# Kernel tuning notes

Hardware: AMD Instinct MI355X
Metric: run time of the kernel (lower is better)

## Reference

```python
import jax, jax.numpy as jnp
import numpy as np

N_GROUPS = 32  # getGroupSize(.) assumed -> channels // 8 (or //24 for 3*ch) == 32 for ch=256
HEADS = 4


def group_norm(x, gamma, beta, groups=N_GROUPS, eps=1e-5):
    n, c = x.shape
    xg = x.reshape(n, groups, c // groups)
    mu = xg.mean(-1, keepdims=True)
    var = xg.var(-1, keepdims=True)
    xn = ((xg - mu) * jax.lax.rsqrt(var + eps)).reshape(n, c)
    return xn * gamma + beta


def setup_inputs():
    key = jax.random.key(0)
    N, E, CH, HID = 2000, 16000, 256, 256
    ks = jax.random.split(key, 24)

    def w(k, shape, s=0.02):
        return (jax.random.normal(k, shape) * s).astype(jnp.float32)

    inp = {
        'x': jax.random.normal(ks[0], (N, CH), jnp.float32),
        'edge_index': jax.random.randint(ks[1], (2, E), 0, N),
        'edge_attr': jax.random.normal(ks[2], (E, CH), jnp.float32),
        # edge_mlp: GN(3ch)+ReLU -> Linear(3ch,hid) -> GN(hid)+ReLU -> Linear(hid,ch)
        'gn_e1_g': jnp.ones((3 * CH,), jnp.float32), 'gn_e1_b': jnp.zeros((3 * CH,), jnp.float32),
        'We1': w(ks[3], (3 * CH, HID)), 'be1': jnp.zeros((HID,), jnp.float32),
        'gn_e2_g': jnp.ones((HID,), jnp.float32), 'gn_e2_b': jnp.zeros((HID,), jnp.float32),
        'We2': w(ks[4], (HID, CH)), 'be2': jnp.zeros((CH,), jnp.float32),
        # actN: GN(ch)+ReLU
        'gn_n_g': jnp.ones((CH,), jnp.float32), 'gn_n_b': jnp.zeros((CH,), jnp.float32),
        # multi-head attention projections
        'Wq': w(ks[5], (CH, CH)), 'bq': jnp.zeros((CH,), jnp.float32),
        'Wk': w(ks[6], (CH, CH)), 'bk': jnp.zeros((CH,), jnp.float32),
        'Wv': w(ks[7], (CH, CH)), 'bv': jnp.zeros((CH,), jnp.float32),
        'Wo': w(ks[8], (CH, CH)), 'bo': jnp.zeros((CH,), jnp.float32),
        # node_mlp: Linear(2ch,hid) -> GN(hid)+ReLU -> Linear(hid,ch)
        'Wn1': w(ks[9], (2 * CH, HID)), 'bn1': jnp.zeros((HID,), jnp.float32),
        'gn_n2_g': jnp.ones((HID,), jnp.float32), 'gn_n2_b': jnp.zeros((HID,), jnp.float32),
        'Wn2': w(ks[10], (HID, CH)), 'bn2': jnp.zeros((CH,), jnp.float32),
    }
    return inp


def reference(x, edge_index, edge_attr,
              gn_e1_g, gn_e1_b, We1, be1, gn_e2_g, gn_e2_b, We2, be2,
              gn_n_g, gn_n_b, Wq, bq, Wk, bk, Wv, bv, Wo, bo,
              Wn1, bn1, gn_n2_g, gn_n2_b, Wn2, bn2):
    row, col = edge_index[0], edge_index[1]
    N, ch = x.shape
    E = edge_attr.shape[0]
    dk = ch // HEADS

    # ---- edge model: cat(src, tgt, e) -> GN/ReLU -> Lin -> GN/ReLU -> Lin (+res) ----
    e_in = jnp.concatenate([x[row], x[col], edge_attr], axis=1)  # [E, 3ch]
    h = jax.nn.relu(group_norm(e_in, gn_e1_g, gn_e1_b))
    h = h @ We1 + be1
    h = jax.nn.relu(group_norm(h, gn_e2_g, gn_e2_b))
    e_out = h @ We2 + be2 + edge_attr  # [E, ch]

    # ---- node model: dense-masked MHA, queries=nodes, keys/values=edges ----
    mask = jnp.zeros((N, E), x.dtype).at[col, jnp.arange(E)].set(1.0)  # scatter adjacency
    q = (x @ Wq + bq).reshape(N, HEADS, dk)
    k = (e_out @ Wk + bk).reshape(E, HEADS, dk)
    v = (e_out @ Wv + bv).reshape(E, HEADS, dk)
    scores = jnp.einsum('nhd,ehd->hne', q, k) / jnp.sqrt(jnp.float32(dk))  # [H, N, E]
    scores = jnp.where(mask[None] > 0, scores, jnp.float32(-1e9))
    attn = jax.nn.softmax(scores, axis=-1)
    g = jnp.einsum('hne,ehd->nhd', attn, v).reshape(N, ch) @ Wo + bo  # [N, ch]

    xa = jax.nn.relu(group_norm(x, gn_n_g, gn_n_b))
    h = jnp.concatenate([xa, g], axis=1) @ Wn1 + bn1  # thinker='cat'
    h = jax.nn.relu(group_norm(h, gn_n2_g, gn_n2_b))
    n_out = h @ Wn2 + bn2 + x  # residual

    return n_out, e_out
```

## Files before the change

### kernel.cpp

```cpp
#include <hip/hip_runtime.h>
#include <hip/hip_bf16.h>
#include <stdint.h>
#include <math.h>

#define CH 256

typedef __attribute__((ext_vector_type(8)))  short short8;
typedef __attribute__((ext_vector_type(16))) short short16;
typedef __attribute__((ext_vector_type(4)))  float f32x4;

#define GL2LDS16(g, l) __builtin_amdgcn_global_load_lds(                       \
    (const __attribute__((address_space(1))) void*)(g),                        \
    (__attribute__((address_space(3))) void*)(l), 16, 0, 0)

__device__ inline short f2bf(float f) {
    __hip_bfloat16 h = __float2bfloat16(f);
    short s;
    __builtin_memcpy(&s, &h, 2);
    return s;
}

__device__ inline float warp_sum64(float v) {
    v += __shfl_xor(v, 32, 64);
    v += __shfl_xor(v, 16, 64);
    v += __shfl_xor(v, 8, 64);
    v += __shfl_xor(v, 4, 64);
    v += __shfl_xor(v, 2, 64);
    v += __shfl_xor(v, 1, 64);
    return v;
}

__device__ inline float warp_max64(float v) {
    v = fmaxf(v, __shfl_xor(v, 32, 64));
    v = fmaxf(v, __shfl_xor(v, 16, 64));
    v = fmaxf(v, __shfl_xor(v, 8, 64));
    v = fmaxf(v, __shfl_xor(v, 4, 64));
    v = fmaxf(v, __shfl_xor(v, 2, 64));
    v = fmaxf(v, __shfl_xor(v, 1, 64));
    return v;
}

template <int BM, int BN, int EPI, int VB>
__global__ __launch_bounds__(256) void mfma_gemm(
    const short* __restrict__ A, const short* __restrict__ Bt,
    const float* __restrict__ bias, const float* __restrict__ res,
    float* __restrict__ C, short* __restrict__ Cbf,
    const float* __restrict__ gamma, const float* __restrict__ beta,
    float* __restrict__ vbar,
    int M, int K, int Nc, int ldc, int coff)
{
    constexpr int BK = 64;
    constexpr int HM = BM / 2, HN = BN / 2;
    constexpr int FM = HM / 16, FN = HN / 16;
    constexpr int PA = (BM * BK) / (256 * 8);
    constexpr int PB = (BN * BK) / (256 * 8);
    __shared__ short As[BM * BK];
    __shared__ short Bs[BN * BK];

    const int t = threadIdx.x;
    const int wave = t >> 6, lane = t & 63;
    const int q = lane >> 4, l16 = lane & 15;
    const int row0 = blockIdx.y * BM;
    const int col0 = blockIdx.x * BN;
    const int wm = wave & 1, wn = wave >> 1;

    f32x4 acc[FM][FN];
    #pragma unroll
    for (int i = 0; i < FM; i++)
        #pragma unroll
        for (int j = 0; j < FN; j++) acc[i][j] = (f32x4){0.f, 0.f, 0.f, 0.f};

    for (int k0 = 0; k0 < K; k0 += BK) {
        #pragma unroll
        for (int p = 0; p < PA; p++) {
            int chunk = p * 256 + t;
            int r = chunk >> 3, ko = (chunk & 7) * 8;
            int gr = row0 + r; if (gr >= M) gr = M - 1;
            const short* gsrc = A + (size_t)gr * K + k0 + ko;
            short* ldst = &As[(p * 256 + wave * 64) * 8];
            GL2LDS16(gsrc, ldst);
        }
        #pragma unroll
        for (int p = 0; p < PB; p++) {
            int chunk = p * 256 + t;
            int r = chunk >> 3, ko = (chunk & 7) * 8;
            const short* gsrc = Bt + (size_t)(col0 + r) * K + k0 + ko;
            short* ldst = &Bs[(p * 256 + wave * 64) * 8];
            GL2LDS16(gsrc, ldst);
        }
        __syncthreads();
        #pragma unroll
        for (int ks = 0; ks < 2; ks++) {
            short8 af[FM], bf[FN];
            #pragma unroll
            for (int mi = 0; mi < FM; mi++)
                af[mi] = *(const short8*)&As[(wm * HM + mi * 16 + l16) * BK + ks * 32 + q * 8];
            #pragma unroll
            for (int ni = 0; ni < FN; ni++)
                bf[ni] = *(const short8*)&Bs[(wn * HN + ni * 16 + l16) * BK + ks * 32 + q * 8];
            #pragma unroll
            for (int mi = 0; mi < FM; mi++)
                #pragma unroll
                for (int ni = 0; ni < FN; ni++)
                    acc[mi][ni] = __builtin_amdgcn_mfma_f32_16x16x32_bf16(
                        af[mi], bf[ni], acc[mi][ni], 0, 0, 0);
        }
        __syncthreads();
    }

    #pragma unroll
    for (int ni = 0; ni < FN; ni++) {
        int cg = col0 + wn * HN + ni * 16 + l16;
        float bv = bias[cg];
        if constexpr (EPI == 1) {
            float ga = gamma[cg], be = beta[cg];
            #pragma unroll
            for (int mi = 0; mi < FM; mi++) {
                #pragma unroll
                for (int r = 0; r < 4; r++) {
                    float v = acc[mi][ni][r] + bv;
                    float s = v, sq = v * v;
                    s += __shfl_xor(s, 1, 64);  sq += __shfl_xor(sq, 1, 64);
                    s += __shfl_xor(s, 2, 64);  sq += __shfl_xor(sq, 2, 64);
                    s += __shfl_xor(s, 4, 64);  sq += __shfl_xor(sq, 4, 64);
                    float mean = s * 0.125f;
                    float var = sq * 0.125f - mean * mean;
                    float o = fmaxf((v - mean) * rsqrtf(var + 1e-5f) * ga + be, 0.f);
                    int rg = row0 + wm * HM + mi * 16 + q * 4 + r;
                    if (rg < M) Cbf[(size_t)rg * ldc + coff + cg] = f2bf(o);
                }
            }
        } else {
            #pragma unroll
            for (int mi = 0; mi < FM; mi++) {
                #pragma unroll
                for (int r = 0; r < 4; r++) {
                    int rg = row0 + wm * HM + mi * 16 + q * 4 + r;
                    if (rg < M) {
                        float v = acc[mi][ni][r] + bv;
                        if (res) v += res[(size_t)rg * ldc + coff + cg];
                        if (C)   C[(size_t)rg * ldc + coff + cg] = v;
                        if (Cbf) Cbf[(size_t)rg * ldc + coff + cg] = f2bf(v);
                    }
                }
            }
            if constexpr (VB) {
                if (cg >= 256) {
                    float part = 0.f;
                    #pragma unroll
                    for (int mi = 0; mi < FM; mi++)
                        #pragma unroll
                        for (int r = 0; r < 4; r++) {
                            int rg = row0 + wm * HM + mi * 16 + q * 4 + r;
                            if (rg < M) part += acc[mi][ni][r] + bv;
                        }
                    part += __shfl_xor(part, 16, 64);
                    part += __shfl_xor(part, 32, 64);
                    if (q == 0) atomicAdd(&vbar[cg - 256], part);
                }
            }
        }
    }
}

struct PrepPack {
    const float* wsrc[8];
    short* wdst[8];
    int wK[8];
    int wstart[8];
    int NW, NP;
    const float* x;
    short* x_bf;
    short* cat_bf;
    const float* gng;
    const float* gnb;
    float* vbar;
    const float* bk;
    const float* bv;
    float* bkv;
    int* counts;
    int N;
};

__global__ __launch_bounds__(256) void prep_kernel(PrepPack p)
{
    int bid = blockIdx.x;
    int t = threadIdx.x;
    if (bid < p.NW) {
        int m = 0;
        #pragma unroll
        for (int i = 1; i < 8; i++) if (bid >= p.wstart[i]) m = i;
        int k0 = (bid - p.wstart[m]) * 16;
        const float* src = p.wsrc[m];
        short16 o;
        #pragma unroll
        for (int j = 0; j < 16; j++) o[j] = f2bf(src[(size_t)(k0 + j) * 256 + t]);
        *(short16*)(p.wdst[m] + (size_t)t * p.wK[m] + k0) = o;
        return;
    }
    if (bid >= p.NW + p.NP) {
        int i = (bid - p.NW - p.NP) * 256 + t;
        if (i < p.N) p.counts[i] = 0;
        return;
    }
    int pb = bid - p.NW;
    if (pb == 0) {
        p.vbar[t] = 0.f;
        p.bkv[t] = p.bk[t];
        p.bkv[256 + t] = p.bv[t];
    }
    int r = pb * 8 + (t >> 5);
    int g = t & 31;
    if (r >= p.N) return;
    size_t xb = (size_t)r * CH + g * 8;
    float4 a = *(const float4*)&p.x[xb];
    float4 b = *(const float4*)&p.x[xb + 4];
    short8 xr;
    xr[0] = f2bf(a.x); xr[1] = f2bf(a.y); xr[2] = f2bf(a.z); xr[3] = f2bf(a.w);
    xr[4] = f2bf(b.x); xr[5] = f2bf(b.y); xr[6] = f2bf(b.z); xr[7] = f2bf(b.w);
    *(short8*)&p.x_bf[xb] = xr;
    float s  = a.x + a.y + a.z + a.w + b.x + b.y + b.z + b.w;
    float s2 = a.x*a.x + a.y*a.y + a.z*a.z + a.w*a.w
             + b.x*b.x + b.y*b.y + b.z*b.z + b.w*b.w;
    float m = s * 0.125f;
    float var = s2 * 0.125f - m * m;
    float rsd = rsqrtf(var + 1e-5f);
    float4 g0 = *(const float4*)&p.gng[g * 8];
    float4 g1 = *(const float4*)&p.gng[g * 8 + 4];
    float4 b0 = *(const float4*)&p.gnb[g * 8];
    float4 b1 = *(const float4*)&p.gnb[g * 8 + 4];
    short8 o;
    o[0] = f2bf(fmaxf((a.x - m) * rsd * g0.x + b0.x, 0.f));
    o[1] = f2bf(fmaxf((a.y - m) * rsd * g0.y + b0.y, 0.f));
    o[2] = f2bf(fmaxf((a.z - m) * rsd * g0.z + b0.z, 0.f));
    o[3] = f2bf(fmaxf((a.w - m) * rsd * g0.w + b0.w, 0.f));
    o[4] = f2bf(fmaxf((b.x - m) * rsd * g1.x + b1.x, 0.f));
    o[5] = f2bf(fmaxf((b.y - m) * rsd * g1.y + b1.y, 0.f));
    o[6] = f2bf(fmaxf((b.z - m) * rsd * g1.z + b1.z, 0.f));
    o[7] = f2bf(fmaxf((b.w - m) * rsd * g1.w + b1.w, 0.f));
    *(short8*)&p.cat_bf[(size_t)r * (2 * CH) + g * 8] = o;
}

__global__ __launch_bounds__(256) void build_ein_kernel(
    const float* __restrict__ x, const float* __restrict__ eattr,
    const int* __restrict__ rowi, const int* __restrict__ coli,
    const float* __restrict__ gng, const float* __restrict__ gnb,
    short* __restrict__ ein, int* __restrict__ counts, int E)
{
    __shared__ float sb[768];
    __shared__ float smu[32], srs[32];
    int e = blockIdx.x, t = threadIdx.x;
    int r = rowi[e], c = coli[e];
    if (t == 0) atomicAdd(&counts[c], 1);
    float v0 = x[(size_t)r * CH + t];
    float v1 = x[(size_t)c * CH + t];
    float v2 = eattr[(size_t)e * CH + t];
    sb[t] = v0; sb[256 + t] = v1; sb[512 + t] = v2;
    __syncthreads();
    if (t < 32) {
        float s = 0.f, s2 = 0.f;
        const float* p = &sb[t * 24];
        #pragma unroll
        for (int i = 0; i < 24; i++) { float v = p[i]; s += v; s2 += v * v; }
        float m = s * (1.f / 24.f);
        float var = s2 * (1.f / 24.f) - m * m;
        smu[t] = m; srs[t] = rsqrtf(var + 1e-5f);
    }
    __syncthreads();
    size_t base = (size_t)e * 768;
    #pragma unroll
    for (int j = 0; j < 3; j++) {
        int pos = j * 256 + t;
        int g = pos / 24;
        float v = (j == 0) ? v0 : (j == 1) ? v1 : v2;
        v = fmaxf((v - smu[g]) * srs[g] * gng[pos] + gnb[pos], 0.f);
        ein[base + pos] = f2bf(v);
    }
}

__global__ __launch_bounds__(1024) void scan_kernel(
    const int* __restrict__ counts, int* __restrict__ offsets,
    int* __restrict__ cursor, int N)
{
    __shared__ int s[1024];
    int t = threadIdx.x;
    int a = (2 * t     < N) ? counts[2 * t]     : 0;
    int b = (2 * t + 1 < N) ? counts[2 * t + 1] : 0;
    s[t] = a + b;
    __syncthreads();
    for (int off = 1; off < 1024; off <<= 1) {
        int v = (t >= off) ? s[t - off] : 0;
        __syncthreads();
        s[t] += v;
        __syncthreads();
    }
    int excl = (t > 0) ? s[t - 1] : 0;
    if (2 * t < N)     { offsets[2 * t]     = excl;     cursor[2 * t]     = excl; }
    if (2 * t + 1 < N) { offsets[2 * t + 1] = excl + a; cursor[2 * t + 1] = excl + a; }
    if (t == 1023) offsets[N] = s[1023];
}

__global__ void fill_kernel(const int* __restrict__ coli, int* __restrict__ cursor,
                            int* __restrict__ elist, int E)
{
    int e = blockIdx.x * blockDim.x + threadIdx.x;
    if (e < E) {
        int p = atomicAdd(&cursor[coli[e]], 1);
        elist[p] = e;
    }
}

__global__ __launch_bounds__(256) void escore_kernel(
    const float* __restrict__ qb, const float* __restrict__ kv,
    const int* __restrict__ coli, float* __restrict__ sc, int E)
{
    int e = blockIdx.x * 4 + (threadIdx.x >> 6);
    int lane = threadIdx.x & 63;
    if (e >= E) return;
    int c = coli[e];
    const float* qrow = qb + (size_t)c * CH;
    const float* krow = kv + (size_t)e * 512;
    float d0 = qrow[lane]       * krow[lane];
    float d1 = qrow[64 + lane]  * krow[64 + lane];
    float d2 = qrow[128 + lane] * krow[128 + lane];
    float d3 = qrow[192 + lane] * krow[192 + lane];
    d0 = warp_sum64(d0);
    d1 = warp_sum64(d1);
    d2 = warp_sum64(d2);
    d3 = warp_sum64(d3);
    if (lane == 0) {
        float4 o = {d0 * 0.125f, d1 * 0.125f, d2 * 0.125f, d3 * 0.125f};
        *(float4*)&sc[(size_t)e * 4] = o;
    }
}

__global__ __launch_bounds__(256) void attn_kernel(
    const float* __restrict__ sc, const float* __restrict__ kv,
    const int* __restrict__ offsets, const int* __restrict__ elist,
    const float* __restrict__ vbar, short* __restrict__ g_bf, int N, int E)
{
    int n = blockIdx.x;
    int h = threadIdx.x >> 6;
    int lane = threadIdx.x & 63;
    int s0 = offsets[n], s1 = offsets[n + 1];
    float out = 0.f;
    if (s1 > s0) {
        float m = -INFINITY, l = 0.f;
        for (int base = s0; base < s1; base += 64) {
            int cn = s1 - base; if (cn > 64) cn = 64;
            int e = (lane < cn) ? elist[base + lane] : 0;
            float s = (lane < cn) ? sc[(size_t)e * 4 + h] : -INFINITY;
            float mc = warp_max64(s);
            float nm = fmaxf(m, mc);
            float scale = __expf(m - nm);
            float pp = (lane < cn) ? __expf(s - nm) : 0.f;
            float ps = warp_sum64(pp);
            l = l * scale + ps;
            out *= scale;
            m = nm;
            for (int i = 0; i < cn; i++) {
                float pi = __shfl(pp, i, 64);
                int   ei = __shfl(e, i, 64);
                out += pi * kv[(size_t)ei * 512 + 256 + h * 64 + lane];
            }
        }
        out /= l;
    } else {
        out = vbar[h * 64 + lane] * (1.f / (float)E);
    }
    g_bf[(size_t)n * CH + h * 64 + lane] = f2bf(out);
}

extern "C" void kernel_launch(void* const* d_in, const int* in_sizes, int n_in,
                              void* d_out, int out_size, void* d_ws, size_t ws_size,
                              hipStream_t stream)
{
    const float* x       = (const float*)d_in[0];
    const int*   ei      = (const int*)d_in[1];
    const float* eattr   = (const float*)d_in[2];
    const float* gn_e1_g = (const float*)d_in[3];
    const float* gn_e1_b = (const float*)d_in[4];
    const float* We1     = (const float*)d_in[5];
    const float* be1     = (const float*)d_in[6];
    const float* gn_e2_g = (const float*)d_in[7];
    const float* gn_e2_b = (const float*)d_in[8];
    const float* We2     = (const float*)d_in[9];
    const float* be2     = (const float*)d_in[10];
    const float* gn_n_g  = (const float*)d_in[11];
    const float* gn_n_b  = (const float*)d_in[12];
    const float* Wq      = (const float*)d_in[13];
    const float* bq      = (const float*)d_in[14];
    const float* Wk      = (const float*)d_in[15];
    const float* bk      = (const float*)d_in[16];
    const float* Wv      = (const float*)d_in[17];
    const float* bv      = (const float*)d_in[18];
    const float* Wo      = (const float*)d_in[19];
    const float* bo      = (const float*)d_in[20];
    const float* Wn1     = (const float*)d_in[21];
    const float* bn1     = (const float*)d_in[22];
    const float* gn_n2_g = (const float*)d_in[23];
    const float* gn_n2_b = (const float*)d_in[24];
    const float* Wn2     = (const float*)d_in[25];
    const float* bn2     = (const float*)d_in[26];

    const int N = in_sizes[0] / CH;
    const int E = in_sizes[2] / CH;

    float* nout = (float*)d_out;
    float* eout = (float*)d_out + (size_t)N * CH;

    char* base = (char*)d_ws;
    short* ein_bf = (short*)base;
    float* kvbuf  = (float*)base;
    base += (size_t)E * 512 * 4;
    short* h2_bf  = (short*)base; base += (size_t)E * CH * 2;
    short* eo_bf  = (short*)base; base += (size_t)E * CH * 2;
    float* qbuf   = (float*)base; base += (size_t)N * CH * 4;
    short* g_bf   = (short*)base; base += (size_t)N * CH * 2;
    short* cat_bf = (short*)base; base += (size_t)N * 2 * CH * 2;
    short* hn_bf  = (short*)base; base += (size_t)N * CH * 2;
    short* x_bf   = (short*)base; base += (size_t)N * CH * 2;
    float* sc     = (float*)base; base += (size_t)E * 4 * 4;
    float* vbar   = (float*)base; base += 1024;
    float* bkv    = (float*)base; base += 2048;
    short* We1t = (short*)base; base += (size_t)768 * 256 * 2;
    short* We2t = (short*)base; base += (size_t)256 * 256 * 2;
    short* Wqt  = (short*)base; base += (size_t)256 * 256 * 2;
    short* Wkvt = (short*)base; base += (size_t)512 * 256 * 2;
    short* Wot  = (short*)base; base += (size_t)256 * 256 * 2;
    short* Wn1t = (short*)base; base += (size_t)512 * 256 * 2;
    short* Wn2t = (short*)base; base += (size_t)256 * 256 * 2;
    int* counts  = (int*)base;
    int* offsets = counts + N;
    int* cursor  = offsets + (N + 1) + 3;
    int* elist   = cursor + N;

    const int* rowi = ei;
    const int* coli = ei + E;

    dim3 blk(256);
    dim3 gE(CH / 64, E / 128);
    dim3 gKV(512 / 128, E / 128);
    dim3 gN(CH / 64, (N + 63) / 64);

    PrepPack pp;
    const float* wsrc[8] = {We1, We2, Wq, Wk, Wv, Wo, Wn1, Wn2};
    short* wdst[8] = {We1t, We2t, Wqt, Wkvt, Wkvt + (size_t)256 * 256, Wot, Wn1t, Wn2t};
    const int wKd[8] = {768, 256, 256, 256, 256, 256, 512, 256};
    int acc = 0;
    for (int i = 0; i < 8; i++) {
        pp.wsrc[i] = wsrc[i]; pp.wdst[i] = wdst[i]; pp.wK[i] = wKd[i];
        pp.wstart[i] = acc; acc += wKd[i] / 16;
    }
    pp.NW = acc;
    pp.NP = (N + 7) / 8;
    pp.x = x; pp.x_bf = x_bf; pp.cat_bf = cat_bf;
    pp.gng = gn_n_g; pp.gnb = gn_n_b;
    pp.vbar = vbar; pp.bk = bk; pp.bv = bv; pp.bkv = bkv;
    pp.counts = counts; pp.N = N;
    int nzero = (N + 255) / 256;
    prep_kernel<<<pp.NW + pp.NP + nzero, blk, 0, stream>>>(pp);

    build_ein_kernel<<<E, blk, 0, stream>>>(x, eattr, rowi, coli, gn_e1_g, gn_e1_b,
                                            ein_bf, counts, E);
    scan_kernel<<<1, 1024, 0, stream>>>(counts, offsets, cursor, N);
    fill_kernel<<<(E + 255) / 256, blk, 0, stream>>>(coli, cursor, elist, E);

    mfma_gemm<128, 64, 1, 0><<<gE, blk, 0, stream>>>(
        ein_bf, We1t, be1, nullptr, nullptr, h2_bf, gn_e2_g, gn_e2_b, nullptr,
        E, 3 * CH, CH, CH, 0);
    mfma_gemm<128, 64, 0, 0><<<gE, blk, 0, stream>>>(
        h2_bf, We2t, be2, eattr, eout, eo_bf, nullptr, nullptr, nullptr,
        E, CH, CH, CH, 0);

    mfma_gemm<128, 128, 0, 1><<<gKV, blk, 0, stream>>>(
        eo_bf, Wkvt, bkv, nullptr, kvbuf, nullptr, nullptr, nullptr, vbar,
        E, CH, 512, 512, 0);
    mfma_gemm<64, 64, 0, 0><<<gN, blk, 0, stream>>>(
        x_bf, Wqt, bq, nullptr, qbuf, nullptr, nullptr, nullptr, nullptr,
        N, CH, CH, CH, 0);

    escore_kernel<<<(E + 3) / 4, blk, 0, stream>>>(qbuf, kvbuf, coli, sc, E);
    attn_kernel<<<N, blk, 0, stream>>>(sc, kvbuf, offsets, elist, vbar, g_bf, N, E);
    mfma_gemm<64, 64, 0, 0><<<gN, blk, 0, stream>>>(
        g_bf, Wot, bo, nullptr, nullptr, cat_bf, nullptr, nullptr, nullptr,
        N, CH, CH, 2 * CH, CH);

    mfma_gemm<64, 64, 1, 0><<<gN, blk, 0, stream>>>(
        cat_bf, Wn1t, bn1, nullptr, nullptr, hn_bf, gn_n2_g, gn_n2_b, nullptr,
        N, 2 * CH, CH, CH, 0);
    mfma_gemm<64, 64, 0, 0><<<gN, blk, 0, stream>>>(
        hn_bf, Wn2t, bn2, x, nout, nullptr, nullptr, nullptr, nullptr,
        N, CH, CH, CH, 0);
}
```

Measured before the change: 267.2 us.

## Fuse edge GroupNorm gather into GEMM A-load, merge Q/KV GEMMs, store KV/Q as bf16

Removes the materialised [E,768] bf16 edge-input buffer. Per-group statistics are now computed from precomputed node partial sums plus edge sums, and the first edge GEMM gathers x rows and eattr, normalizes them and writes the result to LDS itself. The Q and KV projections run as one dual-role launch, and Q/KV are stored in bf16 instead of fp32. The fill kernel is folded into escore. All GEMMs now use 128x128 tiles. This saves memory traffic and launches, but the A tile is now built by a register path instead of async LDS loads, bf16 Q/K adds precision loss, and small-N GEMMs get fewer blocks.

Result: slower. 342.0 us (+28.0%).

```diff
diff --git a/kernel.cpp b/kernel.cpp
--- a/kernel.cpp
+++ b/kernel.cpp
@@ -18,6 +18,13 @@
     short s;
     __builtin_memcpy(&s, &h, 2);
     return s;
+}
+
+__device__ inline float bf2f(short s) {
+    unsigned u = ((unsigned)(unsigned short)s) << 16;
+    float f;
+    __builtin_memcpy(&f, &u, 4);
+    return f;
 }
 
 __device__ inline float warp_sum64(float v) {
@@ -40,48 +47,114 @@
     return v;
 }
 
-template <int BM, int BN, int EPI, int VB>
-__global__ __launch_bounds__(256) void mfma_gemm(
-    const short* __restrict__ A, const short* __restrict__ Bt,
-    const float* __restrict__ bias, const float* __restrict__ res,
-    float* __restrict__ C, short* __restrict__ Cbf,
-    const float* __restrict__ gamma, const float* __restrict__ beta,
-    float* __restrict__ vbar,
-    int M, int K, int Nc, int ldc, int coff)
-{
-    constexpr int BK = 64;
-    constexpr int HM = BM / 2, HN = BN / 2;
-    constexpr int FM = HM / 16, FN = HN / 16;
-    constexpr int PA = (BM * BK) / (256 * 8);
-    constexpr int PB = (BN * BK) / (256 * 8);
-    __shared__ short As[BM * BK];
+struct GArgs {
+    const short* A; const short* Bt; const float* bias; const float* res;
+    float* C; short* Cbf;
+    const float* gamma; const float* beta; float* vbar;
+    int M, K, Nc, ldc, coff;
+    const short* A2; const short* Bt2; const float* bias2; short* Cbf2;
+    int M2, Nc2, y_split;
+    const float* x; const float* eattr; const int* rowi; const int* coli;
+    const float* mu; const float* rs; const float* vg; const float* vbt;
+};
+
+template <int AMODE, int EPI, int DUAL, int VB>
+__global__ __launch_bounds__(256) void mfma_gemm(GArgs g)
+{
+    constexpr int BM = 128, BN = 128, BK = 64;
+    constexpr int AK = AMODE ? (BK + 8) : BK;
+    __shared__ short As[BM * AK];
     __shared__ short Bs[BN * BK];
+    __shared__ int sidx[AMODE ? 256 : 1];
+
+    const short* A = g.A; const short* Bt = g.Bt;
+    const float* bias = g.bias; const float* res = g.res;
+    float* C = g.C; short* Cbf = g.Cbf;
+    int M = g.M, ldc = g.ldc, co = g.coff;
+    const int K = g.K;
+    int by = blockIdx.y, bx = blockIdx.x;
+    bool qrole = false;
+    if constexpr (DUAL) {
+        if (by >= g.y_split) {
+            by -= g.y_split;
+            if (bx * BN >= g.Nc2) return;
+            qrole = true;
+            A = g.A2; Bt = g.Bt2; bias = g.bias2; Cbf = g.Cbf2;
+            C = nullptr; res = nullptr;
+            M = g.M2; ldc = g.Nc2; co = 0;
+        }
+    }
 
     const int t = threadIdx.x;
     const int wave = t >> 6, lane = t & 63;
     const int q = lane >> 4, l16 = lane & 15;
-    const int row0 = blockIdx.y * BM;
-    const int col0 = blockIdx.x * BN;
+    const int row0 = by * BM;
+    const int col0 = bx * BN;
     const int wm = wave & 1, wn = wave >> 1;
 
-    f32x4 acc[FM][FN];
+    if constexpr (AMODE) {
+        if (t < 128) {
+            int gr = row0 + t; if (gr >= M) gr = M - 1;
+            sidx[t] = g.rowi[gr];
+            sidx[128 + t] = g.coli[gr];
+        }
+        __syncthreads();
+    }
+
+    f32x4 acc[4][4];
     #pragma unroll
-    for (int i = 0; i < FM; i++)
+    for (int i = 0; i < 4; i++)
         #pragma unroll
-        for (int j = 0; j < FN; j++) acc[i][j] = (f32x4){0.f, 0.f, 0.f, 0.f};
+        for (int j = 0; j < 4; j++) acc[i][j] = (f32x4){0.f, 0.f, 0.f, 0.f};
 
     for (int k0 = 0; k0 < K; k0 += BK) {
+        if constexpr (AMODE == 1) {
+            int reg = k0 >> 8;
+            int rloc = t >> 3;
+            int cpos = (t & 7) * 8;
+            int pos = k0 + cpos;
+            int G = pos / 24;
+            float4 ga  = *(const float4*)&g.vg[pos];
+            float4 ga2 = *(const float4*)&g.vg[pos + 4];
+            float4 gb  = *(const float4*)&g.vbt[pos];
+            float4 gb2 = *(const float4*)&g.vbt[pos + 4];
+            int off = pos & 255;
+            #pragma unroll
+            for (int p = 0; p < 4; p++) {
+                int rr2 = p * 32 + rloc;
+                int e = row0 + rr2; if (e >= M) e = M - 1;
+                const float* srow;
+                if (reg == 0)      srow = g.x + (size_t)sidx[rr2] * CH;
+                else if (reg == 1) srow = g.x + (size_t)sidx[128 + rr2] * CH;
+                else               srow = g.eattr + (size_t)e * CH;
+                float4 va = *(const float4*)&srow[off];
+                float4 vb4 = *(const float4*)&srow[off + 4];
+                float mm = g.mu[(size_t)e * 32 + G];
+                float rr = g.rs[(size_t)e * 32 + G];
+                short8 o;
+                o[0] = f2bf(fmaxf((va.x - mm) * rr * ga.x + gb.x, 0.f));
+                o[1] = f2bf(fmaxf((va.y - mm) * rr * ga.y + gb.y, 0.f));
+                o[2] = f2bf(fmaxf((va.z - mm) * rr * ga.z + gb.z, 0.f));
+                o[3] = f2bf(fmaxf((va.w - mm) * rr * ga.w + gb.w, 0.f));
+                o[4] = f2bf(fmaxf((vb4.x - mm) * rr * ga2.x + gb2.x, 0.f));
+                o[5] = f2bf(fmaxf((vb4.y - mm) * rr * ga2.y + gb2.y, 0.f));
+                o[6] = f2bf(fmaxf((vb4.z - mm) * rr * ga2.z + gb2.z, 0.f));
+                o[7] = f2bf(fmaxf((vb4.w - mm) * rr * ga2.w + gb2.w, 0.f));
+                *(short8*)&As[rr2 * AK + cpos] = o;
+            }
+        } else {
+            #pragma unroll
+            for (int p = 0; p < 4; p++) {
+                int chunk = p * 256 + t;
+                int r = chunk >> 3, ko = (chunk & 7) * 8;
+                int gr = row0 + r; if (gr >= M) gr = M - 1;
+                const short* gsrc = A + (size_t)gr * K + k0 + ko;
+                short* ldst = &As[(p * 256 + wave * 64) * 8];
+                GL2LDS16(gsrc, ldst);
+            }
+        }
         #pragma unroll
-        for (int p = 0; p < PA; p++) {
-            int chunk = p * 256 + t;
-            int r = chunk >> 3, ko = (chunk & 7) * 8;
-            int gr = row0 + r; if (gr >= M) gr = M - 1;
-            const short* gsrc = A + (size_t)gr * K + k0 + ko;
-            short* ldst = &As[(p * 256 + wave * 64) * 8];
-            GL2LDS16(gsrc, ldst);
-        }
-        #pragma unroll
-        for (int p = 0; p < PB; p++) {
+        for (int p = 0; p < 4; p++) {
             int chunk = p * 256 + t;
             int r = chunk >> 3, ko = (chunk & 7) * 8;
             const short* gsrc = Bt + (size_t)(col0 + r) * K + k0 + ko;
@@ -91,17 +164,17 @@
         __syncthreads();
         #pragma unroll
         for (int ks = 0; ks < 2; ks++) {
-            short8 af[FM], bf[FN];
-            #pragma unroll
-            for (int mi = 0; mi < FM; mi++)
-                af[mi] = *(const short8*)&As[(wm * HM + mi * 16 + l16) * BK + ks * 32 + q * 8];
-            #pragma unroll
-            for (int ni = 0; ni < FN; ni++)
-                bf[ni] = *(const short8*)&Bs[(wn * HN + ni * 16 + l16) * BK + ks * 32 + q * 8];
-            #pragma unroll
-            for (int mi = 0; mi < FM; mi++)
+            short8 af[4], bf[4];
+            #pragma unroll
+            for (int mi = 0; mi < 4; mi++)
+                af[mi] = *(const short8*)&As[(wm * 64 + mi * 16 + l16) * AK + ks * 32 + q * 8];
+            #pragma unroll
+            for (int ni = 0; ni < 4; ni++)
+                bf[ni] = *(const short8*)&Bs[(wn * 64 + ni * 16 + l16) * BK + ks * 32 + q * 8];
+            #pragma unroll
+            for (int mi = 0; mi < 4; mi++)
                 #pragma unroll
-                for (int ni = 0; ni < FN; ni++)
+                for (int ni = 0; ni < 4; ni++)
                     acc[mi][ni] = __builtin_amdgcn_mfma_f32_16x16x32_bf16(
                         af[mi], bf[ni], acc[mi][ni], 0, 0, 0);
         }
@@ -109,13 +182,13 @@
     }
 
     #pragma unroll
-    for (int ni = 0; ni < FN; ni++) {
-        int cg = col0 + wn * HN + ni * 16 + l16;
+    for (int ni = 0; ni < 4; ni++) {
+        int cg = col0 + wn * 64 + ni * 16 + l16;
         float bv = bias[cg];
         if constexpr (EPI == 1) {
-            float ga = gamma[cg], be = beta[cg];
-            #pragma unroll
-            for (int mi = 0; mi < FM; mi++) {
+            float ga = g.gamma[cg], be = g.beta[cg];
+            #pragma unroll
+            for (int mi = 0; mi < 4; mi++) {
                 #pragma unroll
                 for (int r = 0; r < 4; r++) {
                     float v = acc[mi][ni][r] + bv;
@@ -126,37 +199,37 @@
                     float mean = s * 0.125f;
                     float var = sq * 0.125f - mean * mean;
                     float o = fmaxf((v - mean) * rsqrtf(var + 1e-5f) * ga + be, 0.f);
-                    int rg = row0 + wm * HM + mi * 16 + q * 4 + r;
-                    if (rg < M) Cbf[(size_t)rg * ldc + coff + cg] = f2bf(o);
+                    int rg = row0 + wm * 64 + mi * 16 + q * 4 + r;
+                    if (rg < M) Cbf[(size_t)rg * ldc + co + cg] = f2bf(o);
                 }
             }
         } else {
             #pragma unroll
-            for (int mi = 0; mi < FM; mi++) {
+            for (int mi = 0; mi < 4; mi++) {
                 #pragma unroll
                 for (int r = 0; r < 4; r++) {
-                    int rg = row0 + wm * HM + mi * 16 + q * 4 + r;
+                    int rg = row0 + wm * 64 + mi * 16 + q * 4 + r;
                     if (rg < M) {
                         float v = acc[mi][ni][r] + bv;
-                        if (res) v += res[(size_t)rg * ldc + coff + cg];
-                        if (C)   C[(size_t)rg * ldc + coff + cg] = v;
-                        if (Cbf) Cbf[(size_t)rg * ldc + coff + cg] = f2bf(v);
+                        if (res) v += res[(size_t)rg * ldc + co + cg];
+                        if (C)   C[(size_t)rg * ldc + co + cg] = v;
+                        if (Cbf) Cbf[(size_t)rg * ldc + co + cg] = f2bf(v);
                     }
                 }
             }
             if constexpr (VB) {
-                if (cg >= 256) {
+                if (!qrole && cg >= 256) {
                     float part = 0.f;
                     #pragma unroll
-                    for (int mi = 0; mi < FM; mi++)
+                    for (int mi = 0; mi < 4; mi++)
                         #pragma unroll
                         for (int r = 0; r < 4; r++) {
-                            int rg = row0 + wm * HM + mi * 16 + q * 4 + r;
+                            int rg = row0 + wm * 64 + mi * 16 + q * 4 + r;
                             if (rg < M) part += acc[mi][ni][r] + bv;
                         }
                     part += __shfl_xor(part, 16, 64);
                     part += __shfl_xor(part, 32, 64);
-                    if (q == 0) atomicAdd(&vbar[cg - 256], part);
+                    if (q == 0) atomicAdd(&g.vbar[cg - 256], part);
                 }
             }
         }
@@ -172,6 +245,7 @@
     const float* x;
     short* x_bf;
     short* cat_bf;
+    float2* xs;
     const float* gng;
     const float* gnb;
     float* vbar;
@@ -222,6 +296,7 @@
     float s  = a.x + a.y + a.z + a.w + b.x + b.y + b.z + b.w;
     float s2 = a.x*a.x + a.y*a.y + a.z*a.z + a.w*a.w
              + b.x*b.x + b.y*b.y + b.z*b.z + b.w*b.w;
+    p.xs[(size_t)r * 32 + g] = make_float2(s, s2);
     float m = s * 0.125f;
     float var = s2 * 0.125f - m * m;
     float rsd = rsqrtf(var + 1e-5f);
@@ -241,41 +316,40 @@
     *(short8*)&p.cat_bf[(size_t)r * (2 * CH) + g * 8] = o;
 }
 
-__global__ __launch_bounds__(256) void build_ein_kernel(
-    const float* __restrict__ x, const float* __restrict__ eattr,
-    const int* __restrict__ rowi, const int* __restrict__ coli,
-    const float* __restrict__ gng, const float* __restrict__ gnb,
-    short* __restrict__ ein, int* __restrict__ counts, int E)
-{
-    __shared__ float sb[768];
-    __shared__ float smu[32], srs[32];
-    int e = blockIdx.x, t = threadIdx.x;
+__global__ __launch_bounds__(256) void estats_kernel(
+    const float* __restrict__ eattr, const int* __restrict__ rowi,
+    const int* __restrict__ coli, const float2* __restrict__ xs,
+    float* __restrict__ mu, float* __restrict__ rs,
+    int* __restrict__ counts, int E)
+{
+    __shared__ float2 ea[8][32];
+    int t = threadIdx.x;
+    int slot = t >> 5, g = t & 31;
+    int e = blockIdx.x * 8 + slot;
+    float4 a = *(const float4*)&eattr[(size_t)e * CH + g * 8];
+    float4 b = *(const float4*)&eattr[(size_t)e * CH + g * 8 + 4];
+    float s  = a.x + a.y + a.z + a.w + b.x + b.y + b.z + b.w;
+    float s2 = a.x*a.x + a.y*a.y + a.z*a.z + a.w*a.w
+             + b.x*b.x + b.y*b.y + b.z*b.z + b.w*b.w;
+    ea[slot][g] = make_float2(s, s2);
     int r = rowi[e], c = coli[e];
-    if (t == 0) atomicAdd(&counts[c], 1);
-    float v0 = x[(size_t)r * CH + t];
-    float v1 = x[(size_t)c * CH + t];
-    float v2 = eattr[(size_t)e * CH + t];
-    sb[t] = v0; sb[256 + t] = v1; sb[512 + t] = v2;
+    if (g == 0) atomicAdd(&counts[c], 1);
     __syncthreads();
-    if (t < 32) {
-        float s = 0.f, s2 = 0.f;
-        const float* p = &sb[t * 24];
-        #pragma unroll
-        for (int i = 0; i < 24; i++) { float v = p[i]; s += v; s2 += v * v; }
-        float m = s * (1.f / 24.f);
-        float var = s2 * (1.f / 24.f) - m * m;
-        smu[t] = m; srs[t] = rsqrtf(var + 1e-5f);
-    }
-    __syncthreads();
-    size_t base = (size_t)e * 768;
+    float S = 0.f, S2 = 0.f;
     #pragma unroll
     for (int j = 0; j < 3; j++) {
-        int pos = j * 256 + t;
-        int g = pos / 24;
-        float v = (j == 0) ? v0 : (j == 1) ? v1 : v2;
-        v = fmaxf((v - smu[g]) * srs[g] * gng[pos] + gnb[pos], 0.f);
-        ein[base + pos] = f2bf(v);
-    }
+        int b3 = 3 * g + j;
+        int src = b3 >> 5, idx = b3 & 31;
+        float2 v;
+        if (src == 0)      v = xs[(size_t)r * 32 + idx];
+        else if (src == 1) v = xs[(size_t)c * 32 + idx];
+        else               v = ea[slot][idx];
+        S += v.x; S2 += v.y;
+    }
+    float m = S * (1.f / 24.f);
+    float var = S2 * (1.f / 24.f) - m * m;
+    mu[(size_t)e * 32 + g] = m;
+    rs[(size_t)e * 32 + g] = rsqrtf(var + 1e-5f);
 }
 
 __global__ __launch_bounds__(1024) void scan_kernel(
@@ -300,30 +374,22 @@
     if (t == 1023) offsets[N] = s[1023];
 }
 
-__global__ void fill_kernel(const int* __restrict__ coli, int* __restrict__ cursor,
-                            int* __restrict__ elist, int E)
-{
-    int e = blockIdx.x * blockDim.x + threadIdx.x;
-    if (e < E) {
-        int p = atomicAdd(&cursor[coli[e]], 1);
-        elist[p] = e;
-    }
-}
-
 __global__ __launch_bounds__(256) void escore_kernel(
-    const float* __restrict__ qb, const float* __restrict__ kv,
-    const int* __restrict__ coli, float* __restrict__ sc, int E)
+    const short* __restrict__ qb, const short* __restrict__ kvb,
+    const int* __restrict__ coli, int* __restrict__ cursor,
+    int* __restrict__ elist, float* __restrict__ sc, int E)
 {
     int e = blockIdx.x * 4 + (threadIdx.x >> 6);
     int lane = threadIdx.x & 63;
     if (e >= E) return;
     int c = coli[e];
-    const float* qrow = qb + (size_t)c * CH;
-    const float* krow = kv + (size_t)e * 512;
-    float d0 = qrow[lane]       * krow[lane];
-    float d1 = qrow[64 + lane]  * krow[64 + lane];
-    float d2 = qrow[128 + lane] * krow[128 + lane];
-    float d3 = qrow[192 + lane] * krow[192 + lane];
+    if (lane == 0) { int p = atomicAdd(&cursor[c], 1); elist[p] = e; }
+    const short* qrow = qb + (size_t)c * CH;
+    const short* krow = kvb + (size_t)e * 512;
+    float d0 = bf2f(qrow[lane])       * bf2f(krow[lane]);
+    float d1 = bf2f(qrow[64 + lane])  * bf2f(krow[64 + lane]);
+    float d2 = bf2f(qrow[128 + lane]) * bf2f(krow[128 + lane]);
+    float d3 = bf2f(qrow[192 + lane]) * bf2f(krow[192 + lane]);
     d0 = warp_sum64(d0);
     d1 = warp_sum64(d1);
     d2 = warp_sum64(d2);
@@ -335,7 +401,7 @@
 }
 
 __global__ __launch_bounds__(256) void attn_kernel(
-    const float* __restrict__ sc, const float* __restrict__ kv,
+    const float* __restrict__ sc, const short* __restrict__ kvb,
     const int* __restrict__ offsets, const int* __restrict__ elist,
     const float* __restrict__ vbar, short* __restrict__ g_bf, int N, int E)
 {
@@ -361,7 +427,7 @@
             for (int i = 0; i < cn; i++) {
                 float pi = __shfl(pp, i, 64);
                 int   ei = __shfl(e, i, 64);
-                out += pi * kv[(size_t)ei * 512 + 256 + h * 64 + lane];
+                out += pi * bf2f(kvb[(size_t)ei * 512 + 256 + h * 64 + lane]);
             }
         }
         out /= l;
@@ -410,16 +476,17 @@
     float* eout = (float*)d_out + (size_t)N * CH;
 
     char* base = (char*)d_ws;
-    short* ein_bf = (short*)base;
-    float* kvbuf  = (float*)base;
-    base += (size_t)E * 512 * 4;
+    short* kv_bf  = (short*)base; base += (size_t)E * 512 * 2;
     short* h2_bf  = (short*)base; base += (size_t)E * CH * 2;
     short* eo_bf  = (short*)base; base += (size_t)E * CH * 2;
-    float* qbuf   = (float*)base; base += (size_t)N * CH * 4;
+    short* q_bf   = (short*)base; base += (size_t)N * CH * 2;
     short* g_bf   = (short*)base; base += (size_t)N * CH * 2;
     short* cat_bf = (short*)base; base += (size_t)N * 2 * CH * 2;
     short* hn_bf  = (short*)base; base += (size_t)N * CH * 2;
     short* x_bf   = (short*)base; base += (size_t)N * CH * 2;
+    float2* xs    = (float2*)base; base += (size_t)N * 32 * 8;
+    float* mub    = (float*)base; base += (size_t)E * 32 * 4;
+    float* rsb    = (float*)base; base += (size_t)E * 32 * 4;
     float* sc     = (float*)base; base += (size_t)E * 4 * 4;
     float* vbar   = (float*)base; base += 1024;
     float* bkv    = (float*)base; base += 2048;
@@ -439,9 +506,6 @@
     const int* coli = ei + E;
 
     dim3 blk(256);
-    dim3 gE(CH / 64, E / 128);
-    dim3 gKV(512 / 128, E / 128);
-    dim3 gN(CH / 64, (N + 63) / 64);
 
     PrepPack pp;
     const float* wsrc[8] = {We1, We2, Wq, Wk, Wv, Wo, Wn1, Wn2};
@@ -454,42 +518,53 @@
     }
     pp.NW = acc;
     pp.NP = (N + 7) / 8;
-    pp.x = x; pp.x_bf = x_bf; pp.cat_bf = cat_bf;
+    pp.x = x; pp.x_bf = x_bf; pp.cat_bf = cat_bf; pp.xs = xs;
     pp.gng = gn_n_g; pp.gnb = gn_n_b;
     pp.vbar = vbar; pp.bk = bk; pp.bv = bv; pp.bkv = bkv;
     pp.counts = counts; pp.N = N;
     int nzero = (N + 255) / 256;
     prep_kernel<<<pp.NW + pp.NP + nzero, blk, 0, stream>>>(pp);
 
-    build_ein_kernel<<<E, blk, 0, stream>>>(x, eattr, rowi, coli, gn_e1_g, gn_e1_b,
-                                            ein_bf, counts, E);
+    estats_kernel<<<E / 8, blk, 0, stream>>>(eattr, rowi, coli, xs, mub, rsb, counts, E);
     scan_kernel<<<1, 1024, 0, stream>>>(counts, offsets, cursor, N);
-    fill_kernel<<<(E + 255) / 256, blk, 0, stream>>>(coli, cursor, elist, E);
-
-    mfma_gemm<128, 64, 1, 0><<<gE, blk, 0, stream>>>(
-        ein_bf, We1t, be1, nullptr, nullptr, h2_bf, gn_e2_g, gn_e2_b, nullptr,
-        E, 3 * CH, CH, CH, 0);
-    mfma_gemm<128, 64, 0, 0><<<gE, blk, 0, stream>>>(
-        h2_bf, We2t, be2, eattr, eout, eo_bf, nullptr, nullptr, nullptr,
-        E, CH, CH, CH, 0);
-
-    mfma_gemm<128, 128, 0, 1><<<gKV, blk, 0, stream>>>(
-        eo_bf, Wkvt, bkv, nullptr, kvbuf, nullptr, nullptr, nullptr, vbar,
-        E, CH, 512, 512, 0);
-    mfma_gemm<64, 64, 0, 0><<<gN, blk, 0, stream>>>(
-        x_bf, Wqt, bq, nullptr, qbuf, nullptr, nullptr, nullptr, nullptr,
-        N, CH, CH, CH, 0);
-
-    escore_kernel<<<(E + 3) / 4, blk, 0, stream>>>(qbuf, kvbuf, coli, sc, E);
-    attn_kernel<<<N, blk, 0, stream>>>(sc, kvbuf, offsets, elist, vbar, g_bf, N, E);
-    mfma_gemm<64, 64, 0, 0><<<gN, blk, 0, stream>>>(
-        g_bf, Wot, bo, nullptr, nullptr, cat_bf, nullptr, nullptr, nullptr,
-        N, CH, CH, 2 * CH, CH);
-
-    mfma_gemm<64, 64, 1, 0><<<gN, blk, 0, stream>>>(
-        cat_bf, Wn1t, bn1, nullptr, nullptr, hn_bf, gn_n2_g, gn_n2_b, nullptr,
-        N, 2 * CH, CH, CH, 0);
-    mfma_gemm<64, 64, 0, 0><<<gN, blk, 0, stream>>>(
-        hn_bf, Wn2t, bn2, x, nout, nullptr, nullptr, nullptr, nullptr,
-        N, CH, CH, CH, 0);
-}
+
+    GArgs ga = {};
+    ga.Bt = We1t; ga.bias = be1; ga.Cbf = h2_bf;
+    ga.gamma = gn_e2_g; ga.beta = gn_e2_b;
+    ga.M = E; ga.K = 3 * CH; ga.Nc = CH; ga.ldc = CH; ga.coff = 0;
+    ga.x = x; ga.eattr = eattr; ga.rowi = rowi; ga.coli = coli;
+    ga.mu = mub; ga.rs = rsb; ga.vg = gn_e1_g; ga.vbt = gn_e1_b;
+    mfma_gemm<1, 1, 0, 0><<<dim3(2, E / 128), blk, 0, stream>>>(ga);
+
+    ga = {};
+    ga.A = h2_bf; ga.Bt = We2t; ga.bias = be2; ga.res = eattr;
+    ga.C = eout; ga.Cbf = eo_bf;
+    ga.M = E; ga.K = CH; ga.Nc = CH; ga.ldc = CH; ga.coff = 0;
+    mfma_gemm<0, 0, 0, 0><<<dim3(2, E / 128), blk, 0, stream>>>(ga);
+
+    ga = {};
+    ga.A = eo_bf; ga.Bt = Wkvt; ga.bias = bkv; ga.Cbf = kv_bf; ga.vbar = vbar;
+    ga.M = E; ga.K = CH; ga.Nc = 512; ga.ldc = 512; ga.coff = 0;
+    ga.A2 = x_bf; ga.Bt2 = Wqt; ga.bias2 = bq; ga.Cbf2 = q_bf;
+    ga.M2 = N; ga.Nc2 = CH; ga.y_split = E / 128;
+    mfma_gemm<0, 0, 1, 1><<<dim3(4, E / 128 + (N + 127) / 128), blk, 0, stream>>>(ga);
+
+    escore_kernel<<<(E + 3) / 4, blk, 0, stream>>>(q_bf, kv_bf, coli, cursor, elist, sc, E);
+    attn_kernel<<<N, blk, 0, stream>>>(sc, kv_bf, offsets, elist, vbar, g_bf, N, E);
+
+    ga = {};
+    ga.A = g_bf; ga.Bt = Wot; ga.bias = bo; ga.Cbf = cat_bf;
+    ga.M = N; ga.K = CH; ga.Nc = CH; ga.ldc = 2 * CH; ga.coff = CH;
+    mfma_gemm<0, 0, 0, 0><<<dim3(2, (N + 127) / 128), blk, 0, stream>>>(ga);
+
+    ga = {};
+    ga.A = cat_bf; ga.Bt = Wn1t; ga.bias = bn1; ga.Cbf = hn_bf;
+    ga.gamma = gn_n2_g; ga.beta = gn_n2_b;
+    ga.M = N; ga.K = 2 * CH; ga.Nc = CH; ga.ldc = CH; ga.coff = 0;
+    mfma_gemm<0, 1, 0, 0><<<dim3(2, (N + 127) / 128), blk, 0, stream>>>(ga);
+
+    ga = {};
+    ga.A = hn_bf; ga.Bt = Wn2t; ga.bias = bn2; ga.res = x; ga.C = nout;
+    ga.M = N; ga.K = CH; ga.Nc = CH; ga.ldc = CH; ga.coff = 0;
+    mfma_gemm<0, 0, 0, 0><<<dim3(2, (N + 127) / 128), blk, 0, stream>>>(ga);
+}
```
